# Performance work log

Hardware: AMD Instinct MI355X
Metric: run time of the kernel (lower is better)

## Reference

```python
import jax, jax.numpy as jnp
import numpy as np

N_E, E_DIM, BETA = 1024, 64, 0.25

def setup_inputs() -> dict:
    key = jax.random.key(0)
    k1, k2 = jax.random.split(key)
    z = jax.random.normal(k1, (16, 4096, E_DIM), dtype=jnp.float32)
    embedding = jax.random.uniform(k2, (N_E, E_DIM), dtype=jnp.float32,
                                   minval=-1.0 / 256, maxval=1.0 / 256)
    return {"z": z, "embedding": embedding}

def reference(z, embedding):
    # z: [B, S, D]; embedding: [n_e, D]
    zf = z.reshape(-1, E_DIM)  # [N, D]
    # squared euclidean distances: ||z||^2 + ||e||^2 - 2 z e^T -> [N, n_e]
    d = (jnp.sum(zf * zf, axis=1, keepdims=True)
         + jnp.sum(embedding * embedding, axis=1)
         - 2.0 * jnp.matmul(zf, embedding.T))
    min_encoding_indices = jnp.argmin(d, axis=1)  # [N]
    z_q = embedding[min_encoding_indices].reshape(z.shape)  # [B, S, D]
    sg = jax.lax.stop_gradient
    loss = (jnp.mean((z_q - sg(z)) ** 2)
            + BETA * jnp.mean((sg(z_q) - z) ** 2))
    z_q = z + sg(z_q - z)  # straight-through estimator
    return (loss, z_q, min_encoding_indices)
```

## Files before the change

kernel.cpp:

```cpp
#include <hip/hip_runtime.h>


#define D 64
#define NE 1024
#define SEGS 8
#define CPS 128
#define ROWS 64
#define TPB 512

__global__ __launch_bounds__(TPB, 4) void vq_kernel(const float* __restrict__ z,
                                                    const float* __restrict__ emb,
                                                    float* __restrict__ out_loss,
                                                    float* __restrict__ out_zq,
                                                    float* __restrict__ out_idx,
                                                    float loss_scale) {
    __shared__ float ee_lds[NE];
    __shared__ float smv[SEGS * ROWS];
    __shared__ int   smi[SEGS * ROWS];

    const int tid = threadIdx.x;
    const size_t blockRow = (size_t)blockIdx.x * ROWS;
    const int rrow = tid & (ROWS - 1);
    const int seg  = tid >> 6;

    {
#pragma clang fp contract(off)
#pragma unroll
        for (int cc = 0; cc < 2; ++cc) {
            const int j = tid + cc * TPB;
            const float4* e4 = (const float4*)(emb + ((size_t)j << 6));
            float4 a = e4[0], b = e4[1];
            float r[8];
            r[0] = a.x*a.x; r[1] = a.y*a.y; r[2] = a.z*a.z; r[3] = a.w*a.w;
            r[4] = b.x*b.x; r[5] = b.y*b.y; r[6] = b.z*b.z; r[7] = b.w*b.w;
#pragma unroll
            for (int g = 1; g < 8; ++g) {
                float4 c = e4[2*g], e = e4[2*g + 1];
                r[0] = r[0] + c.x*c.x; r[1] = r[1] + c.y*c.y;
                r[2] = r[2] + c.z*c.z; r[3] = r[3] + c.w*c.w;
                r[4] = r[4] + e.x*e.x; r[5] = r[5] + e.y*e.y;
                r[6] = r[6] + e.z*e.z; r[7] = r[7] + e.w*e.w;
            }
            ee_lds[j] = ((r[0]+r[1]) + (r[2]+r[3])) + ((r[4]+r[5]) + (r[6]+r[7]));
        }
    }

    float zr[D];
    {
        const float4* zrow4 = (const float4*)(z + (blockRow + rrow) * D);
#pragma unroll
        for (int c = 0; c < 16; ++c) {
            float4 v = zrow4[c];
            zr[4*c+0] = v.x; zr[4*c+1] = v.y; zr[4*c+2] = v.z; zr[4*c+3] = v.w;
        }
    }

    float zz;
    {
#pragma clang fp contract(off)
        float r[8];
#pragma unroll
        for (int jj = 0; jj < 8; ++jj) { float t = zr[jj] * zr[jj]; r[jj] = t; }
#pragma unroll
        for (int i = 8; i < 64; i += 8) {
#pragma unroll
            for (int jj = 0; jj < 8; ++jj) { float t = zr[i+jj] * zr[i+jj]; r[jj] = r[jj] + t; }
        }
        zz = ((r[0]+r[1]) + (r[2]+r[3])) + ((r[4]+r[5]) + (r[6]+r[7]));
    }

    __syncthreads();

    float minv = __builtin_inff();
    int mini = 0;
    const int jbase = __builtin_amdgcn_readfirstlane(seg * CPS);
#pragma unroll 2
    for (int jj = 0; jj < CPS; ++jj) {
        const int j = jbase + jj;
        const float4* ew4 = (const float4*)(emb + ((size_t)j << 6));
        float p0 = 0.f, p1 = 0.f, p2 = 0.f, p3 = 0.f;
#pragma unroll
        for (int c = 0; c < 16; ++c) {
            float4 e4 = ew4[c];
            p0 = fmaf(zr[4*c+0], e4.x, p0);
            p1 = fmaf(zr[4*c+1], e4.y, p1);
            p2 = fmaf(zr[4*c+2], e4.z, p2);
            p3 = fmaf(zr[4*c+3], e4.w, p3);
        }
        float dot = (p0 + p1) + (p2 + p3);
        float t1 = zz + ee_lds[j];
        float d = fmaf(-2.0f, dot, t1);
        if (d < minv) { minv = d; mini = j; }
    }

    smv[seg * ROWS + rrow] = minv;
    smi[seg * ROWS + rrow] = mini;
    __syncthreads();

    float best = __builtin_inff();
    int bi = 0;
#pragma unroll
    for (int s = 0; s < SEGS; ++s) {
        float v = smv[s * ROWS + rrow];
        if (v < best) { best = v; bi = smi[s * ROWS + rrow]; }
    }

    const float4* qe4 = (const float4*)(emb + ((size_t)bi << 6));
    float s = 0.f;
    float* orow = out_zq + (blockRow + rrow) * D;
#pragma unroll
    for (int c = 0; c < 16; ++c) {
        float4 q = qe4[c];
        float z0 = zr[4*c+0], z1 = zr[4*c+1], z2 = zr[4*c+2], z3 = zr[4*c+3];
        float d0 = q.x - z0, d1 = q.y - z1, d2 = q.z - z2, d3 = q.w - z3;
        s += d0*d0; s += d1*d1; s += d2*d2; s += d3*d3;
        if ((c >> 1) == seg) {
            orow[4*c+0] = z0 + d0; orow[4*c+1] = z1 + d1;
            orow[4*c+2] = z2 + d2; orow[4*c+3] = z3 + d3;
        }
    }

    if (seg == 0) {
        out_idx[blockRow + rrow] = (float)bi;
#pragma unroll
        for (int off = 32; off; off >>= 1) s += __shfl_down(s, off);
        if (tid == 0) atomicAdd(out_loss, s * loss_scale);
    }
}

extern "C" void kernel_launch(void* const* d_in, const int* in_sizes, int n_in,
                              void* d_out, int out_size, void* d_ws, size_t ws_size,
                              hipStream_t stream) {
    const float* z   = (const float*)d_in[0];
    const float* emb = (const float*)d_in[1];
    const int nz = in_sizes[0];
    const int N  = nz / D;

    float* out      = (float*)d_out;
    float* out_zq   = out + 1;
    float* out_idx  = out + 1 + (size_t)nz;

    const float loss_scale = 1.25f / (float)nz;

    hipMemsetAsync(out, 0, sizeof(float), stream);
    vq_kernel<<<N / ROWS, TPB, 0, stream>>>(z, emb, out, out_zq, out_idx, loss_scale);
}
```

Measured before the change: 254.3 us.

## Swap loop mapping: keep codebook rows in registers, broadcast z rows from LDS

After: 430.9 us. 1.69x slower.

```diff
diff --git a/kernel.cpp b/kernel.cpp
--- a/kernel.cpp
+++ b/kernel.cpp
@@ -4,124 +4,175 @@
 #define D 64
 #define NE 1024
 #define SEGS 8
-#define CPS 128
 #define ROWS 64
 #define TPB 512
 
-__global__ __launch_bounds__(TPB, 4) void vq_kernel(const float* __restrict__ z,
+__global__ __launch_bounds__(TPB, 2) void vq_kernel(const float* __restrict__ z,
                                                     const float* __restrict__ emb,
                                                     float* __restrict__ out_loss,
                                                     float* __restrict__ out_zq,
                                                     float* __restrict__ out_idx,
                                                     float loss_scale) {
-    __shared__ float ee_lds[NE];
+    __shared__ float lds_z[ROWS * D];
+    __shared__ float zz_lds[ROWS];
     __shared__ float smv[SEGS * ROWS];
     __shared__ int   smi[SEGS * ROWS];
 
-    const int tid = threadIdx.x;
+    const int tid  = threadIdx.x;
+    const int lane = tid & 63;
+    const int w    = tid >> 6;
     const size_t blockRow = (size_t)blockIdx.x * ROWS;
-    const int rrow = tid & (ROWS - 1);
-    const int seg  = tid >> 6;
 
     {
+        const float4* zg4 = (const float4*)(z + blockRow * D);
+        float4 v0 = zg4[tid];
+        float4 v1 = zg4[tid + TPB];
+        ((float4*)lds_z)[tid]       = v0;
+        ((float4*)lds_z)[tid + TPB] = v1;
+    }
+
+    const int jA = (w << 7) + lane;
+    const int jB = jA + 64;
+    float4 ea[16], eb[16];
+    {
+        const float4* e4a = (const float4*)(emb + ((size_t)jA << 6));
+        const float4* e4b = (const float4*)(emb + ((size_t)jB << 6));
+#pragma unroll
+        for (int c = 0; c < 16; ++c) ea[c] = e4a[c];
+#pragma unroll
+        for (int c = 0; c < 16; ++c) eb[c] = e4b[c];
+    }
+
+    float eeA, eeB;
+    {
 #pragma clang fp contract(off)
-#pragma unroll
-        for (int cc = 0; cc < 2; ++cc) {
-            const int j = tid + cc * TPB;
-            const float4* e4 = (const float4*)(emb + ((size_t)j << 6));
-            float4 a = e4[0], b = e4[1];
+        {
+            float4 a = ea[0], b = ea[1];
             float r[8];
-            r[0] = a.x*a.x; r[1] = a.y*a.y; r[2] = a.z*a.z; r[3] = a.w*a.w;
-            r[4] = b.x*b.x; r[5] = b.y*b.y; r[6] = b.z*b.z; r[7] = b.w*b.w;
+            r[0]=a.x*a.x; r[1]=a.y*a.y; r[2]=a.z*a.z; r[3]=a.w*a.w;
+            r[4]=b.x*b.x; r[5]=b.y*b.y; r[6]=b.z*b.z; r[7]=b.w*b.w;
 #pragma unroll
             for (int g = 1; g < 8; ++g) {
-                float4 c = e4[2*g], e = e4[2*g + 1];
-                r[0] = r[0] + c.x*c.x; r[1] = r[1] + c.y*c.y;
-                r[2] = r[2] + c.z*c.z; r[3] = r[3] + c.w*c.w;
-                r[4] = r[4] + e.x*e.x; r[5] = r[5] + e.y*e.y;
-                r[6] = r[6] + e.z*e.z; r[7] = r[7] + e.w*e.w;
+                float4 c = ea[2*g], e = ea[2*g+1];
+                r[0]=r[0]+c.x*c.x; r[1]=r[1]+c.y*c.y;
+                r[2]=r[2]+c.z*c.z; r[3]=r[3]+c.w*c.w;
+                r[4]=r[4]+e.x*e.x; r[5]=r[5]+e.y*e.y;
+                r[6]=r[6]+e.z*e.z; r[7]=r[7]+e.w*e.w;
             }
-            ee_lds[j] = ((r[0]+r[1]) + (r[2]+r[3])) + ((r[4]+r[5]) + (r[6]+r[7]));
+            eeA = ((r[0]+r[1])+(r[2]+r[3])) + ((r[4]+r[5])+(r[6]+r[7]));
+        }
+        {
+            float4 a = eb[0], b = eb[1];
+            float r[8];
+            r[0]=a.x*a.x; r[1]=a.y*a.y; r[2]=a.z*a.z; r[3]=a.w*a.w;
+            r[4]=b.x*b.x; r[5]=b.y*b.y; r[6]=b.z*b.z; r[7]=b.w*b.w;
+#pragma unroll
+            for (int g = 1; g < 8; ++g) {
+                float4 c = eb[2*g], e = eb[2*g+1];
+                r[0]=r[0]+c.x*c.x; r[1]=r[1]+c.y*c.y;
+                r[2]=r[2]+c.z*c.z; r[3]=r[3]+c.w*c.w;
+                r[4]=r[4]+e.x*e.x; r[5]=r[5]+e.y*e.y;
+                r[6]=r[6]+e.z*e.z; r[7]=r[7]+e.w*e.w;
+            }
+            eeB = ((r[0]+r[1])+(r[2]+r[3])) + ((r[4]+r[5])+(r[6]+r[7]));
         }
     }
 
-    float zr[D];
-    {
-        const float4* zrow4 = (const float4*)(z + (blockRow + rrow) * D);
+    if (tid < ROWS) {
+        float zr[D];
+        const float4* zrow4 = (const float4*)(z + (blockRow + tid) * D);
 #pragma unroll
         for (int c = 0; c < 16; ++c) {
             float4 v = zrow4[c];
-            zr[4*c+0] = v.x; zr[4*c+1] = v.y; zr[4*c+2] = v.z; zr[4*c+3] = v.w;
+            zr[4*c+0]=v.x; zr[4*c+1]=v.y; zr[4*c+2]=v.z; zr[4*c+3]=v.w;
+        }
+        {
+#pragma clang fp contract(off)
+            float r[8];
+#pragma unroll
+            for (int jj = 0; jj < 8; ++jj) { float t = zr[jj]*zr[jj]; r[jj] = t; }
+#pragma unroll
+            for (int i = 8; i < 64; i += 8) {
+#pragma unroll
+                for (int jj = 0; jj < 8; ++jj) { float t = zr[i+jj]*zr[i+jj]; r[jj] = r[jj] + t; }
+            }
+            zz_lds[tid] = ((r[0]+r[1])+(r[2]+r[3])) + ((r[4]+r[5])+(r[6]+r[7]));
         }
     }
-
-    float zz;
-    {
-#pragma clang fp contract(off)
-        float r[8];
-#pragma unroll
-        for (int jj = 0; jj < 8; ++jj) { float t = zr[jj] * zr[jj]; r[jj] = t; }
-#pragma unroll
-        for (int i = 8; i < 64; i += 8) {
-#pragma unroll
-            for (int jj = 0; jj < 8; ++jj) { float t = zr[i+jj] * zr[i+jj]; r[jj] = r[jj] + t; }
-        }
-        zz = ((r[0]+r[1]) + (r[2]+r[3])) + ((r[4]+r[5]) + (r[6]+r[7]));
-    }
-
     __syncthreads();
 
-    float minv = __builtin_inff();
-    int mini = 0;
-    const int jbase = __builtin_amdgcn_readfirstlane(seg * CPS);
 #pragma unroll 2
-    for (int jj = 0; jj < CPS; ++jj) {
-        const int j = jbase + jj;
-        const float4* ew4 = (const float4*)(emb + ((size_t)j << 6));
-        float p0 = 0.f, p1 = 0.f, p2 = 0.f, p3 = 0.f;
+    for (int r = 0; r < ROWS; ++r) {
+        const float* zrow = &lds_z[r * D];
+        float zzr = zz_lds[r];
+        float pa0=0.f, pa1=0.f, pa2=0.f, pa3=0.f;
+        float pb0=0.f, pb1=0.f, pb2=0.f, pb3=0.f;
 #pragma unroll
         for (int c = 0; c < 16; ++c) {
-            float4 e4 = ew4[c];
-            p0 = fmaf(zr[4*c+0], e4.x, p0);
-            p1 = fmaf(zr[4*c+1], e4.y, p1);
-            p2 = fmaf(zr[4*c+2], e4.z, p2);
-            p3 = fmaf(zr[4*c+3], e4.w, p3);
+            float4 zc = *(const float4*)&zrow[c * 4];
+            pa0 = fmaf(zc.x, ea[c].x, pa0);
+            pa1 = fmaf(zc.y, ea[c].y, pa1);
+            pa2 = fmaf(zc.z, ea[c].z, pa2);
+            pa3 = fmaf(zc.w, ea[c].w, pa3);
+            pb0 = fmaf(zc.x, eb[c].x, pb0);
+            pb1 = fmaf(zc.y, eb[c].y, pb1);
+            pb2 = fmaf(zc.z, eb[c].z, pb2);
+            pb3 = fmaf(zc.w, eb[c].w, pb3);
         }
-        float dot = (p0 + p1) + (p2 + p3);
-        float t1 = zz + ee_lds[j];
-        float d = fmaf(-2.0f, dot, t1);
-        if (d < minv) { minv = d; mini = j; }
+        float dotA = (pa0 + pa1) + (pa2 + pa3);
+        float dotB = (pb0 + pb1) + (pb2 + pb3);
+        float t1a = zzr + eeA;
+        float t1b = zzr + eeB;
+        float dA = fmaf(-2.0f, dotA, t1a);
+        float dB = fmaf(-2.0f, dotB, t1b);
+
+        float bv = dA; int bj = jA;
+        if (dB < bv) { bv = dB; bj = jB; }
+
+#pragma unroll
+        for (int off = 32; off; off >>= 1) {
+            float ov = __shfl_xor(bv, off);
+            int   oi = __shfl_xor(bj, off);
+            if (ov < bv || (ov == bv && oi < bj)) { bv = ov; bj = oi; }
+        }
+        if (lane == 0) { smv[w * ROWS + r] = bv; smi[w * ROWS + r] = bj; }
     }
-
-    smv[seg * ROWS + rrow] = minv;
-    smi[seg * ROWS + rrow] = mini;
     __syncthreads();
 
+    float zr[D];
+    {
+        const float4* zrow4 = (const float4*)(z + (blockRow + lane) * D);
+#pragma unroll
+        for (int c = 0; c < 16; ++c) {
+            float4 v = zrow4[c];
+            zr[4*c+0]=v.x; zr[4*c+1]=v.y; zr[4*c+2]=v.z; zr[4*c+3]=v.w;
+        }
+    }
     float best = __builtin_inff();
     int bi = 0;
 #pragma unroll
     for (int s = 0; s < SEGS; ++s) {
-        float v = smv[s * ROWS + rrow];
-        if (v < best) { best = v; bi = smi[s * ROWS + rrow]; }
+        float v = smv[s * ROWS + lane];
+        if (v < best) { best = v; bi = smi[s * ROWS + lane]; }
     }
 
     const float4* qe4 = (const float4*)(emb + ((size_t)bi << 6));
     float s = 0.f;
-    float* orow = out_zq + (blockRow + rrow) * D;
+    float* orow = out_zq + (blockRow + lane) * D;
 #pragma unroll
     for (int c = 0; c < 16; ++c) {
         float4 q = qe4[c];
         float z0 = zr[4*c+0], z1 = zr[4*c+1], z2 = zr[4*c+2], z3 = zr[4*c+3];
         float d0 = q.x - z0, d1 = q.y - z1, d2 = q.z - z2, d3 = q.w - z3;
         s += d0*d0; s += d1*d1; s += d2*d2; s += d3*d3;
-        if ((c >> 1) == seg) {
+        if ((c >> 1) == w) {
             orow[4*c+0] = z0 + d0; orow[4*c+1] = z1 + d1;
             orow[4*c+2] = z2 + d2; orow[4*c+3] = z3 + d3;
         }
     }
 
-    if (seg == 0) {
-        out_idx[blockRow + rrow] = (float)bi;
+    if (w == 0) {
+        out_idx[blockRow + lane] = (float)bi;
 #pragma unroll
         for (int off = 32; off; off >>= 1) s += __shfl_down(s, off);
         if (tid == 0) atomicAdd(out_loss, s * loss_scale);
```

## Split VQ into codebook-segmented scan kernel and separate finish kernel

Applied to the files above, without the earlier changes.

Result: slower. 286.3 us (+12.5%).

```diff
diff --git a/kernel.cpp b/kernel.cpp
--- a/kernel.cpp
+++ b/kernel.cpp
@@ -3,55 +3,52 @@
 
 #define D 64
 #define NE 1024
-#define SEGS 8
-#define CPS 128
-#define ROWS 64
-#define TPB 512
+#define NSEG 4
+#define CPS 256
+#define TPB1 256
+#define RPB1 256
+#define TPB2 512
+#define ROWS2 64
 
-__global__ __launch_bounds__(TPB, 4) void vq_kernel(const float* __restrict__ z,
-                                                    const float* __restrict__ emb,
-                                                    float* __restrict__ out_loss,
-                                                    float* __restrict__ out_zq,
-                                                    float* __restrict__ out_idx,
-                                                    float loss_scale) {
-    __shared__ float ee_lds[NE];
-    __shared__ float smv[SEGS * ROWS];
-    __shared__ int   smi[SEGS * ROWS];
+__global__ __launch_bounds__(TPB1, 4) void vq_scan(const float* __restrict__ z,
+                                                   const float* __restrict__ emb,
+                                                   uint2* __restrict__ part,
+                                                   int N) {
+    __shared__ float ee_lds[CPS];
 
-    const int tid = threadIdx.x;
-    const size_t blockRow = (size_t)blockIdx.x * ROWS;
-    const int rrow = tid & (ROWS - 1);
-    const int seg  = tid >> 6;
+    const int tid  = threadIdx.x;
+    const int lane = tid & 63;
+    const int w    = tid >> 6;
+    const int seg  = blockIdx.y;
+    const int jbase0 = seg * CPS;
+    const size_t row = (size_t)blockIdx.x * RPB1 + (size_t)(w << 6) + lane;
 
     {
 #pragma clang fp contract(off)
+        const int j = jbase0 + tid;
+        const float4* e4 = (const float4*)(emb + ((size_t)j << 6));
+        float4 a = e4[0], b = e4[1];
+        float r[8];
+        r[0]=a.x*a.x; r[1]=a.y*a.y; r[2]=a.z*a.z; r[3]=a.w*a.w;
+        r[4]=b.x*b.x; r[5]=b.y*b.y; r[6]=b.z*b.z; r[7]=b.w*b.w;
 #pragma unroll
-        for (int cc = 0; cc < 2; ++cc) {
-            const int j = tid + cc * TPB;
-            const float4* e4 = (const float4*)(emb + ((size_t)j << 6));
-            float4 a = e4[0], b = e4[1];
-            float r[8];
-            r[0] = a.x*a.x; r[1] = a.y*a.y; r[2] = a.z*a.z; r[3] = a.w*a.w;
-            r[4] = b.x*b.x; r[5] = b.y*b.y; r[6] = b.z*b.z; r[7] = b.w*b.w;
-#pragma unroll
-            for (int g = 1; g < 8; ++g) {
-                float4 c = e4[2*g], e = e4[2*g + 1];
-                r[0] = r[0] + c.x*c.x; r[1] = r[1] + c.y*c.y;
-                r[2] = r[2] + c.z*c.z; r[3] = r[3] + c.w*c.w;
-                r[4] = r[4] + e.x*e.x; r[5] = r[5] + e.y*e.y;
-                r[6] = r[6] + e.z*e.z; r[7] = r[7] + e.w*e.w;
-            }
-            ee_lds[j] = ((r[0]+r[1]) + (r[2]+r[3])) + ((r[4]+r[5]) + (r[6]+r[7]));
+        for (int g = 1; g < 8; ++g) {
+            float4 c = e4[2*g], e = e4[2*g + 1];
+            r[0]=r[0]+c.x*c.x; r[1]=r[1]+c.y*c.y;
+            r[2]=r[2]+c.z*c.z; r[3]=r[3]+c.w*c.w;
+            r[4]=r[4]+e.x*e.x; r[5]=r[5]+e.y*e.y;
+            r[6]=r[6]+e.z*e.z; r[7]=r[7]+e.w*e.w;
         }
+        ee_lds[tid] = ((r[0]+r[1])+(r[2]+r[3])) + ((r[4]+r[5])+(r[6]+r[7]));
     }
 
     float zr[D];
     {
-        const float4* zrow4 = (const float4*)(z + (blockRow + rrow) * D);
+        const float4* zrow4 = (const float4*)(z + row * D);
 #pragma unroll
         for (int c = 0; c < 16; ++c) {
             float4 v = zrow4[c];
-            zr[4*c+0] = v.x; zr[4*c+1] = v.y; zr[4*c+2] = v.z; zr[4*c+3] = v.w;
+            zr[4*c+0]=v.x; zr[4*c+1]=v.y; zr[4*c+2]=v.z; zr[4*c+3]=v.w;
         }
     }
 
@@ -60,20 +57,19 @@
 #pragma clang fp contract(off)
         float r[8];
 #pragma unroll
-        for (int jj = 0; jj < 8; ++jj) { float t = zr[jj] * zr[jj]; r[jj] = t; }
+        for (int jj = 0; jj < 8; ++jj) { float t = zr[jj]*zr[jj]; r[jj] = t; }
 #pragma unroll
         for (int i = 8; i < 64; i += 8) {
 #pragma unroll
-            for (int jj = 0; jj < 8; ++jj) { float t = zr[i+jj] * zr[i+jj]; r[jj] = r[jj] + t; }
+            for (int jj = 0; jj < 8; ++jj) { float t = zr[i+jj]*zr[i+jj]; r[jj] = r[jj] + t; }
         }
-        zz = ((r[0]+r[1]) + (r[2]+r[3])) + ((r[4]+r[5]) + (r[6]+r[7]));
+        zz = ((r[0]+r[1])+(r[2]+r[3])) + ((r[4]+r[5])+(r[6]+r[7]));
     }
-
     __syncthreads();
 
     float minv = __builtin_inff();
     int mini = 0;
-    const int jbase = __builtin_amdgcn_readfirstlane(seg * CPS);
+    const int jbase = __builtin_amdgcn_readfirstlane(jbase0);
 #pragma unroll 2
     for (int jj = 0; jj < CPS; ++jj) {
         const int j = jbase + jj;
@@ -88,40 +84,64 @@
             p3 = fmaf(zr[4*c+3], e4.w, p3);
         }
         float dot = (p0 + p1) + (p2 + p3);
-        float t1 = zz + ee_lds[j];
+        float t1 = zz + ee_lds[jj];
         float d = fmaf(-2.0f, dot, t1);
         if (d < minv) { minv = d; mini = j; }
     }
 
-    smv[seg * ROWS + rrow] = minv;
-    smi[seg * ROWS + rrow] = mini;
-    __syncthreads();
+    part[(size_t)seg * (size_t)N + row] = make_uint2(__float_as_uint(minv),
+                                                     (unsigned)mini);
+}
+
+__global__ __launch_bounds__(TPB2, 4) void vq_finish(const float* __restrict__ z,
+                                                     const float* __restrict__ emb,
+                                                     const uint2* __restrict__ part,
+                                                     float* __restrict__ out_loss,
+                                                     float* __restrict__ out_zq,
+                                                     float* __restrict__ out_idx,
+                                                     float loss_scale, int N) {
+    const int tid  = threadIdx.x;
+    const int lane = tid & 63;
+    const int w    = tid >> 6;
+    const size_t blockRow = (size_t)blockIdx.x * ROWS2;
+    const size_t row = blockRow + lane;
 
     float best = __builtin_inff();
     int bi = 0;
 #pragma unroll
-    for (int s = 0; s < SEGS; ++s) {
-        float v = smv[s * ROWS + rrow];
-        if (v < best) { best = v; bi = smi[s * ROWS + rrow]; }
+    for (int s = 0; s < NSEG; ++s) {
+        uint2 p = part[(size_t)s * (size_t)N + row];
+        float v = __uint_as_float(p.x);
+        if (v < best) { best = v; bi = (int)p.y; }
+    }
+
+    float zr[D];
+    {
+        const float4* zrow4 = (const float4*)(z + row * D);
+#pragma unroll
+        for (int c = 0; c < 16; ++c) {
+            float4 v = zrow4[c];
+            zr[4*c+0]=v.x; zr[4*c+1]=v.y; zr[4*c+2]=v.z; zr[4*c+3]=v.w;
+        }
     }
 
     const float4* qe4 = (const float4*)(emb + ((size_t)bi << 6));
     float s = 0.f;
-    float* orow = out_zq + (blockRow + rrow) * D;
+    float* orow = out_zq + row * D;
 #pragma unroll
     for (int c = 0; c < 16; ++c) {
         float4 q = qe4[c];
         float z0 = zr[4*c+0], z1 = zr[4*c+1], z2 = zr[4*c+2], z3 = zr[4*c+3];
         float d0 = q.x - z0, d1 = q.y - z1, d2 = q.z - z2, d3 = q.w - z3;
         s += d0*d0; s += d1*d1; s += d2*d2; s += d3*d3;
-        if ((c >> 1) == seg) {
+        if ((c >> 1) == w) {
             orow[4*c+0] = z0 + d0; orow[4*c+1] = z1 + d1;
             orow[4*c+2] = z2 + d2; orow[4*c+3] = z3 + d3;
         }
     }
 
-    if (seg == 0) {
-        out_idx[blockRow + rrow] = (float)bi;
+    if (w == 0) {
+        out_idx[row] = (float)bi;
 #pragma unroll
         for (int off = 32; off; off >>= 1) s += __shfl_down(s, off);
         if (tid == 0) atomicAdd(out_loss, s * loss_scale);
@@ -139,9 +159,14 @@
     float* out      = (float*)d_out;
     float* out_zq   = out + 1;
     float* out_idx  = out + 1 + (size_t)nz;
+    uint2* part     = (uint2*)d_ws;
 
     const float loss_scale = 1.25f / (float)nz;
 
     hipMemsetAsync(out, 0, sizeof(float), stream);
-    vq_kernel<<<N / ROWS, TPB, 0, stream>>>(z, emb, out, out_zq, out_idx, loss_scale);
+
+    dim3 g1(N / RPB1, NSEG);
+    vq_scan<<<g1, TPB1, 0, stream>>>(z, emb, part, N);
+    vq_finish<<<N / ROWS2, TPB2, 0, stream>>>(z, emb, part, out, out_zq, out_idx,
+                                              loss_scale, N);
 }
```
